# Performance work log

Hardware: AMD Instinct MI355X
Metric: run time of the kernel (lower is better)

The kernel has to match this reference:

```python
import jax, jax.numpy as jnp
import numpy as np

B, T, DEMO = 64, 4096, 8
N_MOD, N_POS = 37, 10
D_IN = N_POS + 1 + N_MOD  # 48
PHI_W, LATENT = 128, 128
PSI_W, PSI_L = 128, 128
DOT, HEADS = 64, 4
RHO_W, OUT = 128, 1
MAX_TIME = 1000.0


def _dense_init(key, fan_in, fan_out):
    lim = float(np.sqrt(6.0 / fan_in))  # he_uniform-ish
    return jax.random.uniform(key, (fan_in, fan_out), jnp.float32, -lim, lim)


def setup_inputs() -> dict:
    key = jax.random.key(0)
    ks = jax.random.split(key, 32)
    inp = {}
    inp['demo'] = jax.random.normal(ks[0], (B, DEMO), jnp.float32)
    inp['times'] = jax.random.uniform(ks[1], (B, T, 1), jnp.float32, 0.0, 100.0)
    inp['values'] = jax.random.normal(ks[2], (B, T, 1), jnp.float32)
    inp['measurements'] = jax.random.randint(ks[3], (B, T), 0, N_MOD, jnp.int32)
    # all sequences full length -> N = B*(T+1) static
    inp['segment_ids'] = jnp.repeat(jnp.arange(B, dtype=jnp.int32), T + 1)
    inp['timescales'] = jnp.asarray(MAX_TIME ** np.linspace(0.0, 1.0, N_POS // 2), jnp.float32)
    inp['demo_W1'] = _dense_init(ks[4], DEMO, PHI_W); inp['demo_b1'] = jnp.zeros((PHI_W,), jnp.float32)
    inp['demo_W2'] = _dense_init(ks[5], PHI_W, D_IN); inp['demo_b2'] = jnp.zeros((D_IN,), jnp.float32)
    dims = [D_IN, PHI_W, PHI_W, PHI_W, LATENT]
    for i in range(4):
        inp['phi_W%d' % i] = _dense_init(ks[6 + i], dims[i], dims[i + 1])
        inp['phi_b%d' % i] = jnp.zeros((dims[i + 1],), jnp.float32)
    pdims = [D_IN, PSI_W, PSI_W, PSI_L]
    for i in range(3):
        inp['psi_W%d' % i] = _dense_init(ks[10 + i], pdims[i], pdims[i + 1])
        inp['psi_b%d' % i] = jnp.zeros((pdims[i + 1],), jnp.float32)
    inp['W_k'] = _dense_init(ks[13], PSI_L + D_IN, DOT * HEADS)
    # original inits W_q to zeros (degenerate uniform attention); small random keeps test non-trivial
    inp['W_q'] = jax.random.normal(ks[14], (HEADS, DOT), jnp.float32) * 0.05
    rdims = [LATENT * HEADS, RHO_W, RHO_W, RHO_W, OUT]
    for i in range(4):
        inp['rho_W%d' % i] = _dense_init(ks[15 + i], rdims[i], rdims[i + 1])
        inp['rho_b%d' % i] = jnp.zeros((rdims[i + 1],), jnp.float32)
    return inp


def _forward(demo, times, values, timescales,
             demo_W1, demo_b1, demo_W2, demo_b2,
             phi_W0, phi_b0, phi_W1, phi_b1, phi_W2, phi_b2, phi_W3, phi_b3,
             psi_W0, psi_b0, psi_W1, psi_b1, psi_W2, psi_b2,
             W_k, W_q,
             rho_W0, rho_b0, rho_W1, rho_b1, rho_W2, rho_b2, rho_W3, rho_b3,
             measurements, segment_ids):
    relu = jax.nn.relu
    nseg = demo.shape[0]
    # positional encoding: times [B,T,1] / timescales [5] -> sin|cos -> [B,T,10]
    scaled = times / timescales[None, None, :]
    tt = jnp.concatenate([jnp.sin(scaled), jnp.cos(scaled)], axis=-1)
    meas = jax.nn.one_hot(measurements, N_MOD, dtype=times.dtype)  # [B,T,37]
    combined = jnp.concatenate([tt, values, meas], axis=-1)        # [B,T,48]
    demo_enc = relu(demo @ demo_W1 + demo_b1) @ demo_W2 + demo_b2  # [B,48]
    x = jnp.concatenate([demo_enc[:, None, :], combined], axis=1)  # [B,T+1,48]
    collected = x.reshape(-1, x.shape[-1])                         # [N,48]
    # phi MLP -> encoded [N,LATENT]
    h = collected
    for W, b in ((phi_W0, phi_b0), (phi_W1, phi_b1), (phi_W2, phi_b2), (phi_W3, phi_b3)):
        h = relu(h @ W + b)
    encoded = h
    # psi MLP -> [N,PSI_L], then per-segment mean, scattered back
    p = collected
    for W, b in ((psi_W0, psi_b0), (psi_W1, psi_b1), (psi_W2, psi_b2)):
        p = relu(p @ W + b)
    seg_sum = jax.ops.segment_sum(p, segment_ids, num_segments=nseg)
    counts = jax.ops.segment_sum(jnp.ones((p.shape[0],), p.dtype), segment_ids, num_segments=nseg)
    agg = seg_sum / counts[:, None]
    comb2 = jnp.concatenate([collected, agg[segment_ids]], axis=-1)  # [N, 48+128]
    keys = (comb2 @ W_k).reshape(-1, HEADS, DOT)                     # [N,H,D]
    preattn = jnp.einsum('nhd,hd->nh', keys, W_q) / jnp.sqrt(jnp.float32(DOT))
    # segment softmax per head
    m = jax.ops.segment_max(preattn, segment_ids, num_segments=nseg)
    e = jnp.exp(preattn - m[segment_ids])
    s = jax.ops.segment_sum(e, segment_ids, num_segments=nseg)
    attn = e / s[segment_ids]                                        # [N,H]
    # head-major weighted concat: [N, H*LATENT]
    weighted = (attn[:, :, None] * encoded[:, None, :]).reshape(-1, HEADS * LATENT)
    agg_out = jax.ops.segment_sum(weighted, segment_ids, num_segments=nseg)  # [B,512]
    r = agg_out
    for W, b in ((rho_W0, rho_b0), (rho_W1, rho_b1), (rho_W2, rho_b2)):
        r = relu(r @ W + b)
    return jax.nn.sigmoid(r @ rho_W3 + rho_b3)  # [B,1]


def reference(demo, times, values, timescales,
              demo_W1, demo_b1, demo_W2, demo_b2,
              phi_W0, phi_b0, phi_W1, phi_b1, phi_W2, phi_b2, phi_W3, phi_b3,
              psi_W0, psi_b0, psi_W1, psi_b1, psi_W2, psi_b2,
              W_k, W_q,
              rho_W0, rho_b0, rho_W1, rho_b1, rho_W2, rho_b2, rho_W3, rho_b3,
              measurements, segment_ids):
    return _forward(demo, times, values, timescales,
                    demo_W1, demo_b1, demo_W2, demo_b2,
                    phi_W0, phi_b0, phi_W1, phi_b1, phi_W2, phi_b2, phi_W3, phi_b3,
                    psi_W0, psi_b0, psi_W1, psi_b1, psi_W2, psi_b2,
                    W_k, W_q,
                    rho_W0, rho_b0, rho_W1, rho_b1, rho_W2, rho_b2, rho_W3, rho_b3,
                    measurements, segment_ids)
```

## Files before the change

### kernel.cpp

```cpp
#include <hip/hip_runtime.h>
#include <hip/hip_bf16.h>
#include <math.h>


#define BSEG 64
#define TLEN 4096
#define NPART 9
#define PART_STRIDE 520

#define OFF_DEMO 0
#define OFF_WQ   3072
#define OFF_WT   3264
#define OFF_PARTIALS 31936

typedef __attribute__((ext_vector_type(8))) short short8;
typedef __attribute__((ext_vector_type(4))) float f32x4;

static __device__ __forceinline__ float bfbits2f(unsigned v) { return __uint_as_float(v << 16); }
static __device__ __forceinline__ unsigned short f2bf_rne(float x) {
  unsigned u = __float_as_uint(x);
  unsigned r = (u + 0x7FFFu + ((u >> 16) & 1u)) >> 16;
  return (unsigned short)r;
}
static __device__ __forceinline__ unsigned pk2(float a, float b) {
  float2 f2 = make_float2(a, b);
  __hip_bfloat162 h = __float22bfloat162_rn(f2);
  unsigned u;
  __builtin_memcpy(&u, &h, 4);
  return u;
}

__global__ __launch_bounds__(256) void k_prep(
    const float* __restrict__ demo, const float* __restrict__ dW1, const float* __restrict__ db1,
    const float* __restrict__ dW2, const float* __restrict__ db2,
    const float* __restrict__ Wk, const float* __restrict__ Wq,
    const float* __restrict__ W0, const float* __restrict__ W1,
    const float* __restrict__ W2, const float* __restrict__ W3,
    float* __restrict__ ws) {
  __shared__ float drow[8];
  __shared__ float hdrow[128];
  int bid = blockIdx.x, tid = threadIdx.x;
  if (bid < 224) {
    unsigned short* wt = (unsigned short*)(ws + OFF_WT);
    int i = bid * 256 + tid;
    float v;
    if (i < 8192) {
      int n = i >> 6, k = i & 63;
      v = (k < 48) ? W0[k * 128 + n] : 0.f;
    } else {
      int j = i - 8192;
      int l = j >> 14, r = j & 16383;
      int n = r >> 7, k = r & 127;
      const float* W = (l == 0) ? W1 : (l == 1) ? W2 : W3;
      v = W[k * 128 + n];
    }
    wt[i] = f2bf_rne(v);
    return;
  }
  if (bid == 224) {
    if (tid < 192) {
      int i = tid >> 2, h = tid & 3;
      float a = 0.f;
      for (int d = 0; d < 64; ++d) a = fmaf(Wk[i * 256 + h * 64 + d], Wq[h * 64 + d], a);
      ws[OFF_WQ + tid] = a * 0.125f;
    }
    return;
  }
  int r = bid - 225;
  if (tid < 8) drow[tid] = demo[r * 8 + tid];
  __syncthreads();
  if (tid < 128) {
    float a = db1[tid];
#pragma unroll
    for (int i = 0; i < 8; ++i) a = fmaf(drow[i], dW1[i * 128 + tid], a);
    hdrow[tid] = fmaxf(a, 0.f);
  }
  __syncthreads();
  if (tid < 48) {
    float a = db2[tid];
    for (int k = 0; k < 128; ++k) a = fmaf(hdrow[k], dW2[k * 48 + tid], a);
    ws[OFF_DEMO + r * 48 + tid] = a;
  }
}

template<int MT>
static __device__ __forceinline__ void mfma_layer_T(
    const unsigned short* hin, unsigned short* hout,
    const short8 (&Wf)[2][4], const f32x4 (&bias4)[2],
    int l16, int quad, int n0) {
#pragma unroll
  for (int mt = 0; mt < MT; ++mt) {
    short8 Bv[4];
#pragma unroll
    for (int s = 0; s < 4; ++s)
      Bv[s] = *(const short8*)(hin + (mt * 16 + l16) * 136 + s * 32 + quad * 8);
    f32x4 a0 = bias4[0], a1 = bias4[1];
#pragma unroll
    for (int s = 0; s < 4; ++s) {
      a0 = __builtin_amdgcn_mfma_f32_16x16x32_bf16(Wf[0][s], Bv[s], a0, 0, 0, 0);
      a1 = __builtin_amdgcn_mfma_f32_16x16x32_bf16(Wf[1][s], Bv[s], a1, 0, 0, 0);
    }
    uint4 o;
    o.x = pk2(fmaxf(a0[0], 0.f), fmaxf(a0[1], 0.f));
    o.y = pk2(fmaxf(a0[2], 0.f), fmaxf(a0[3], 0.f));
    o.z = pk2(fmaxf(a1[0], 0.f), fmaxf(a1[1], 0.f));
    o.w = pk2(fmaxf(a1[2], 0.f), fmaxf(a1[3], 0.f));
    *(uint4*)(hout + (mt * 16 + l16) * 136 + n0 + quad * 8) = o;
  }
}
template<int MT>
static __device__ __forceinline__ void mfma_layer0_T(
    const unsigned short* cin, unsigned short* hout,
    const short8 (&Wf)[2][2], const f32x4 (&bias4)[2],
    int l16, int quad, int n0) {
#pragma unroll
  for (int mt = 0; mt < MT; ++mt) {
    short8 Bv[2];
#pragma unroll
    for (int s = 0; s < 2; ++s)
      Bv[s] = *(const short8*)(cin + (mt * 16 + l16) * 72 + s * 32 + quad * 8);
    f32x4 a0 = bias4[0], a1 = bias4[1];
    a0 = __builtin_amdgcn_mfma_f32_16x16x32_bf16(Wf[0][0], Bv[0], a0, 0, 0, 0);
    a0 = __builtin_amdgcn_mfma_f32_16x16x32_bf16(Wf[0][1], Bv[1], a0, 0, 0, 0);
    a1 = __builtin_amdgcn_mfma_f32_16x16x32_bf16(Wf[1][0], Bv[0], a1, 0, 0, 0);
    a1 = __builtin_amdgcn_mfma_f32_16x16x32_bf16(Wf[1][1], Bv[1], a1, 0, 0, 0);
    uint4 o;
    o.x = pk2(fmaxf(a0[0], 0.f), fmaxf(a0[1], 0.f));
    o.y = pk2(fmaxf(a0[2], 0.f), fmaxf(a0[3], 0.f));
    o.z = pk2(fmaxf(a1[0], 0.f), fmaxf(a1[1], 0.f));
    o.w = pk2(fmaxf(a1[2], 0.f), fmaxf(a1[3], 0.f));
    *(uint4*)(hout + (mt * 16 + l16) * 136 + n0 + quad * 8) = o;
  }
}

__global__ __launch_bounds__(256, 2) void k_main(
    const float* __restrict__ times, const float* __restrict__ values,
    const int* __restrict__ meas, const float* __restrict__ tsc,
    const float* __restrict__ ws,
    const float* __restrict__ b0g, const float* __restrict__ b1g,
    const float* __restrict__ b2g, const float* __restrict__ b3g,
    float* __restrict__ part) {
  __shared__ __align__(16) unsigned short hA[128 * 136];
  __shared__ __align__(16) unsigned short hB[128 * 136];
  __shared__ __align__(16) float preb[512 * 4];
  __shared__ float wql[192];
  __shared__ float mred[16];
  int tid = threadIdx.x;
  const int lane = tid & 63, wv = tid >> 6, quad = lane >> 4, l16 = lane & 15;
  const int n0 = wv * 32;

  const unsigned short* wt = (const unsigned short*)(ws + OFF_WT);
  short8 B0[2][2], B1[2][4], B2[2][4], B3[2][4];
  f32x4 bias0[2], bias1[2], bias2[2];
  float bias3[2];
#pragma unroll
  for (int t = 0; t < 2; ++t) {
    int n  = n0 + ((l16 >> 2) << 3) + t * 4 + (l16 & 3);
    int nq = n0 + quad * 8 + t * 4;
    bias0[t] = *(const f32x4*)(b0g + nq);
    bias1[t] = *(const f32x4*)(b1g + nq);
    bias2[t] = *(const f32x4*)(b2g + nq);
    bias3[t] = b3g[n];
#pragma unroll
    for (int s = 0; s < 2; ++s)
      B0[t][s] = *(const short8*)(wt + n * 64 + s * 32 + quad * 8);
#pragma unroll
    for (int s = 0; s < 4; ++s) {
      B1[t][s] = *(const short8*)(wt + 8192  + n * 128 + s * 32 + quad * 8);
      B2[t][s] = *(const short8*)(wt + 24576 + n * 128 + s * 32 + quad * 8);
      B3[t][s] = *(const short8*)(wt + 40960 + n * 128 + s * 32 + quad * 8);
    }
  }
  if (tid < 192) wql[tid] = ws[OFF_WQ + tid];
  __syncthreads();

  if (blockIdx.x == 512) {
    {
      int r = tid >> 2, cs = tid & 3;
      unsigned short seg[16];
#pragma unroll
      for (int i = 0; i < 16; ++i) seg[i] = 0;
      if (cs < 3)
#pragma unroll
        for (int i = 0; i < 16; ++i) seg[i] = f2bf_rne(ws[OFF_DEMO + r * 48 + cs * 16 + i]);
      unsigned u[8];
#pragma unroll
      for (int i = 0; i < 8; ++i) u[i] = (unsigned)seg[2 * i] | ((unsigned)seg[2 * i + 1] << 16);
      uint4* dst = (uint4*)(hB + r * 72 + cs * 16);
      dst[0] = make_uint4(u[0], u[1], u[2], u[3]);
      dst[1] = make_uint4(u[4], u[5], u[6], u[7]);
    }
    {
      int r = tid >> 2, h = tid & 3;
      float a = 0.f;
      for (int i = 0; i < 48; ++i) a = fmaf(ws[OFF_DEMO + r * 48 + i], wql[i * 4 + h], a);
      preb[tid] = __expf(a);
    }
    f32x4 bias34[2];
#pragma unroll
    for (int t = 0; t < 2; ++t) bias34[t] = *(const f32x4*)(b3g + n0 + quad * 8 + t * 4);
    __syncthreads();
    mfma_layer0_T<4>(hB, hA, B0, bias0, l16, quad, n0); __syncthreads();
    mfma_layer_T<4>(hA, hB, B1, bias1, l16, quad, n0); __syncthreads();
    mfma_layer_T<4>(hB, hA, B2, bias2, l16, quad, n0); __syncthreads();
    mfma_layer_T<4>(hA, hB, B3, bias34, l16, quad, n0); __syncthreads();
    {
      int r = tid >> 2, h = tid & 3;
      part[(r * NPART + 8) * PART_STRIDE + 4 + h] = preb[tid];
    }
    for (int i = tid; i < 64 * 512; i += 256) {
      int r = i >> 9, rem = i & 511;
      int h = rem >> 7, l = rem & 127;
      part[(r * NPART + 8) * PART_STRIDE + 8 + rem] =
          preb[r * 4 + h] * bfbits2f(hB[r * 136 + l]);
    }
    return;
  }

  int b = blockIdx.x >> 3, c = blockIdx.x & 7;
  int t0 = c << 9;
  float invts[5];
#pragma unroll
  for (int i = 0; i < 5; ++i) invts[i] = 1.f / tsc[i];

  float s4[4] = {0.f, 0.f, 0.f, 0.f};
  unsigned usv0[8], usv1[8];
#pragma unroll
  for (int rr = 0; rr < 2; ++rr) {
    int r = tid + rr * 256;
    int t = t0 + r;
    float tv = times[b * TLEN + t];
    float vvv = values[b * TLEN + t];
    int mm = meas[b * TLEN + t];
    float f[11];
#pragma unroll
    for (int i = 0; i < 5; ++i) { float s = tv * invts[i]; f[i] = __sinf(s); f[5 + i] = __cosf(s); }
    f[10] = vvv;
#pragma unroll
    for (int h = 0; h < 4; ++h) {
      float a = wql[(11 + mm) * 4 + h];
#pragma unroll
      for (int i = 0; i < 11; ++i) a = fmaf(f[i], wql[i * 4 + h], a);
      float e = __expf(a);
      preb[r * 4 + h] = e;
      s4[h] += e;
    }
    int kk = 11 + mm;
    unsigned uu[8];
    uu[0] = pk2(f[0], f[1]); uu[1] = pk2(f[2], f[3]);
    uu[2] = pk2(f[4], f[5]); uu[3] = pk2(f[6], f[7]);
    uu[4] = pk2(f[8], f[9]);
    uu[5] = pk2(f[10], (kk == 11) ? 1.f : 0.f);
    uu[6] = ((kk == 12) ? 0x3F80u : 0u) | ((kk == 13) ? 0x3F800000u : 0u);
    uu[7] = ((kk == 14) ? 0x3F80u : 0u) | ((kk == 15) ? 0x3F800000u : 0u);
    if (rr == 0) {
#pragma unroll
      for (int k = 0; k < 8; ++k) usv0[k] = uu[k];
    } else {
#pragma unroll
      for (int k = 0; k < 8; ++k) usv1[k] = uu[k];
    }
  }

  auto build_tile = [&](int tile) {
    int r = tid & 127;
    if (((tid >> 7) & 1) == (tile & 1)) {
      unsigned uw[8];
#pragma unroll
      for (int k = 0; k < 8; ++k) uw[k] = (tile & 2) ? usv1[k] : usv0[k];
      uint4* dst = (uint4*)(hB + r * 72);
      dst[0] = make_uint4(uw[0], uw[1], uw[2], uw[3]);
      dst[1] = make_uint4(uw[4], uw[5], uw[6], uw[7]);
    } else {
      int t = t0 + tile * 128 + r;
      int mm = meas[b * TLEN + t];
      int kk = 11 + mm;
      uint4 z = make_uint4(0u, 0u, 0u, 0u);
      uint4* dst = (uint4*)(hB + r * 72 + 16);
#pragma unroll
      for (int k = 0; k < 6; ++k) dst[k] = z;
      asm volatile("" ::: "memory");
      if (kk >= 16) hB[r * 72 + kk] = 0x3F80;
    }
  };

  float pacc[2][4] = {{0.f, 0.f, 0.f, 0.f}, {0.f, 0.f, 0.f, 0.f}};
  const int ncb = n0 + ((l16 >> 2) << 3) + (l16 & 3);
  build_tile(0);
  for (int tile = 0; tile < 4; ++tile) {
    int rb = tile << 7;
    __syncthreads();
    mfma_layer0_T<8>(hB, hA, B0, bias0, l16, quad, n0); __syncthreads();
    mfma_layer_T<8>(hA, hB, B1, bias1, l16, quad, n0); __syncthreads();
    mfma_layer_T<8>(hB, hA, B2, bias2, l16, quad, n0); __syncthreads();
    if (tile < 3) build_tile(tile + 1);
#pragma unroll
    for (int mt = 0; mt < 8; ++mt) {
      short8 A[4];
#pragma unroll
      for (int s = 0; s < 4; ++s)
        A[s] = *(const short8*)(hA + (mt * 16 + l16) * 136 + s * 32 + quad * 8);
      f32x4 acc0 = {bias3[0], bias3[0], bias3[0], bias3[0]};
      f32x4 acc1 = {bias3[1], bias3[1], bias3[1], bias3[1]};
#pragma unroll
      for (int s = 0; s < 4; ++s) {
        acc0 = __builtin_amdgcn_mfma_f32_16x16x32_bf16(A[s], B3[0][s], acc0, 0, 0, 0);
        acc1 = __builtin_amdgcn_mfma_f32_16x16x32_bf16(A[s], B3[1][s], acc1, 0, 0, 0);
      }
#pragma unroll
      for (int j = 0; j < 4; ++j) {
        int row = rb + mt * 16 + quad * 4 + j;
        float4 e4 = *(const float4*)(preb + row * 4);
        float v0 = fmaxf(acc0[j], 0.f), v1 = fmaxf(acc1[j], 0.f);
        pacc[0][0] = fmaf(v0, e4.x, pacc[0][0]);
        pacc[0][1] = fmaf(v0, e4.y, pacc[0][1]);
        pacc[0][2] = fmaf(v0, e4.z, pacc[0][2]);
        pacc[0][3] = fmaf(v0, e4.w, pacc[0][3]);
        pacc[1][0] = fmaf(v1, e4.x, pacc[1][0]);
        pacc[1][1] = fmaf(v1, e4.y, pacc[1][1]);
        pacc[1][2] = fmaf(v1, e4.z, pacc[1][2]);
        pacc[1][3] = fmaf(v1, e4.w, pacc[1][3]);
      }
    }
  }
#pragma unroll
  for (int t = 0; t < 2; ++t)
#pragma unroll
    for (int h = 0; h < 4; ++h) {
      float v = pacc[t][h];
      v += __shfl_xor(v, 16, 64);
      v += __shfl_xor(v, 32, 64);
      pacc[t][h] = v;
    }
#pragma unroll
  for (int off = 32; off > 0; off >>= 1)
#pragma unroll
    for (int h = 0; h < 4; ++h) s4[h] += __shfl_xor(s4[h], off, 64);
  if (lane == 0)
#pragma unroll
    for (int h = 0; h < 4; ++h) mred[wv * 4 + h] = s4[h];
  __syncthreads();
  float* P = part + (b * NPART + c) * PART_STRIDE;
  if (tid < 4) P[4 + tid] = mred[tid] + mred[4 + tid] + mred[8 + tid] + mred[12 + tid];
  if (quad == 0)
#pragma unroll
    for (int t = 0; t < 2; ++t)
#pragma unroll
      for (int h = 0; h < 4; ++h)
        P[8 + h * 128 + (ncb + t * 4)] = pacc[t][h];
}

__global__ __launch_bounds__(256) void k_combine(
    const float* __restrict__ part,
    const float* __restrict__ rW0, const float* __restrict__ rb0,
    const float* __restrict__ rW1, const float* __restrict__ rb1,
    const float* __restrict__ rW2, const float* __restrict__ rb2,
    const float* __restrict__ rW3, const float* __restrict__ rb3,
    float* __restrict__ out) {
  __shared__ float Ss[4], agg[512], r1[128], p0[256];
  int tid = threadIdx.x;
  int b = blockIdx.x;
  const float* P = part + b * NPART * PART_STRIDE;
  if (tid < 4) {
    float s = 0.f;
    for (int p = 0; p < NPART; ++p) s += P[p * PART_STRIDE + 4 + tid];
    Ss[tid] = s;
  }
  __syncthreads();
  for (int idx = tid; idx < 512; idx += 256) {
    int h = idx >> 7;
    float a = 0.f;
    for (int p = 0; p < NPART; ++p) a += P[p * PART_STRIDE + 8 + idx];
    agg[idx] = a / Ss[h];
  }
  __syncthreads();
  const int col = tid & 127, half = tid >> 7;
  {
    float a = 0.f;
    for (int k = half * 256; k < half * 256 + 256; ++k) a = fmaf(agg[k], rW0[k * 128 + col], a);
    p0[tid] = a;
  }
  __syncthreads();
  if (tid < 128) r1[tid] = fmaxf(rb0[tid] + p0[tid] + p0[128 + tid], 0.f);
  __syncthreads();
  {
    float a = 0.f;
    for (int k = half * 64; k < half * 64 + 64; ++k) a = fmaf(r1[k], rW1[k * 128 + col], a);
    p0[tid] = a;
  }
  __syncthreads();
  if (tid < 128) r1[tid] = fmaxf(rb1[tid] + p0[tid] + p0[128 + tid], 0.f);
  __syncthreads();
  {
    float a = 0.f;
    for (int k = half * 64; k < half * 64 + 64; ++k) a = fmaf(r1[k], rW2[k * 128 + col], a);
    p0[tid] = a;
  }
  __syncthreads();
  if (tid < 128) p0[tid] = fmaxf(rb2[tid] + p0[tid] + p0[128 + tid], 0.f) * rW3[tid];
  __syncthreads();
  if (tid < 64) {
    float v = p0[tid] + p0[tid + 64];
#pragma unroll
    for (int off = 32; off > 0; off >>= 1) v += __shfl_xor(v, off, 64);
    if (tid == 0) out[b] = 1.f / (1.f + __expf(-(rb3[0] + v)));
  }
}

extern "C" void kernel_launch(void* const* d_in, const int* in_sizes, int n_in,
                              void* d_out, int out_size, void* d_ws, size_t ws_size,
                              hipStream_t stream) {
  const float* demo   = (const float*)d_in[0];
  const float* times  = (const float*)d_in[1];
  const float* values = (const float*)d_in[2];
  const int*   meas   = (const int*)d_in[3];
  const float* tsc = (const float*)d_in[5];
  const float* dW1 = (const float*)d_in[6];
  const float* db1 = (const float*)d_in[7];
  const float* dW2 = (const float*)d_in[8];
  const float* db2 = (const float*)d_in[9];
  const float* pW0 = (const float*)d_in[10];
  const float* pb0 = (const float*)d_in[11];
  const float* pW1 = (const float*)d_in[12];
  const float* pb1 = (const float*)d_in[13];
  const float* pW2 = (const float*)d_in[14];
  const float* pb2 = (const float*)d_in[15];
  const float* pW3 = (const float*)d_in[16];
  const float* pb3 = (const float*)d_in[17];
  const float* Wk  = (const float*)d_in[24];
  const float* Wq  = (const float*)d_in[25];
  const float* rW0 = (const float*)d_in[26];
  const float* rb0 = (const float*)d_in[27];
  const float* rW1 = (const float*)d_in[28];
  const float* rb1 = (const float*)d_in[29];
  const float* rW2 = (const float*)d_in[30];
  const float* rb2 = (const float*)d_in[31];
  const float* rW3 = (const float*)d_in[32];
  const float* rb3 = (const float*)d_in[33];
  float* ws = (float*)d_ws;
  float* partials = ws + OFF_PARTIALS;

  k_prep<<<289, 256, 0, stream>>>(demo, dW1, db1, dW2, db2, Wk, Wq,
                                  pW0, pW1, pW2, pW3, ws);
  k_main<<<513, 256, 0, stream>>>(times, values, meas, tsc, ws,
                                  pb0, pb1, pb2, pb3, partials);
  k_combine<<<64, 256, 0, stream>>>(partials, rW0, rb0, rW1, rb1, rW2, rb2, rW3, rb3,
                                    (float*)d_out);
}
```

Measured before the change: 183.1 us.

## Add MFMA priority hints, vectorize epilogues, and trim redundant LDS zeroing

```diff
diff --git a/kernel.cpp b/kernel.cpp
--- a/kernel.cpp
+++ b/kernel.cpp
@@ -15,6 +15,7 @@
 
 typedef __attribute__((ext_vector_type(8))) short short8;
 typedef __attribute__((ext_vector_type(4))) float f32x4;
+typedef __attribute__((ext_vector_type(2))) float f32x2;
 
 static __device__ __forceinline__ float bfbits2f(unsigned v) { return __uint_as_float(v << 16); }
 static __device__ __forceinline__ unsigned short f2bf_rne(float x) {
@@ -88,6 +89,7 @@
     const unsigned short* hin, unsigned short* hout,
     const short8 (&Wf)[2][4], const f32x4 (&bias4)[2],
     int l16, int quad, int n0) {
+  const f32x4 z4 = {0.f, 0.f, 0.f, 0.f};
 #pragma unroll
   for (int mt = 0; mt < MT; ++mt) {
     short8 Bv[4];
@@ -95,16 +97,20 @@
     for (int s = 0; s < 4; ++s)
       Bv[s] = *(const short8*)(hin + (mt * 16 + l16) * 136 + s * 32 + quad * 8);
     f32x4 a0 = bias4[0], a1 = bias4[1];
+    __builtin_amdgcn_s_setprio(1);
 #pragma unroll
     for (int s = 0; s < 4; ++s) {
       a0 = __builtin_amdgcn_mfma_f32_16x16x32_bf16(Wf[0][s], Bv[s], a0, 0, 0, 0);
       a1 = __builtin_amdgcn_mfma_f32_16x16x32_bf16(Wf[1][s], Bv[s], a1, 0, 0, 0);
     }
+    __builtin_amdgcn_s_setprio(0);
+    f32x4 r0 = __builtin_elementwise_max(a0, z4);
+    f32x4 r1 = __builtin_elementwise_max(a1, z4);
     uint4 o;
-    o.x = pk2(fmaxf(a0[0], 0.f), fmaxf(a0[1], 0.f));
-    o.y = pk2(fmaxf(a0[2], 0.f), fmaxf(a0[3], 0.f));
-    o.z = pk2(fmaxf(a1[0], 0.f), fmaxf(a1[1], 0.f));
-    o.w = pk2(fmaxf(a1[2], 0.f), fmaxf(a1[3], 0.f));
+    o.x = pk2(r0[0], r0[1]);
+    o.y = pk2(r0[2], r0[3]);
+    o.z = pk2(r1[0], r1[1]);
+    o.w = pk2(r1[2], r1[3]);
     *(uint4*)(hout + (mt * 16 + l16) * 136 + n0 + quad * 8) = o;
   }
 }
@@ -113,6 +119,7 @@
     const unsigned short* cin, unsigned short* hout,
     const short8 (&Wf)[2][2], const f32x4 (&bias4)[2],
     int l16, int quad, int n0) {
+  const f32x4 z4 = {0.f, 0.f, 0.f, 0.f};
 #pragma unroll
   for (int mt = 0; mt < MT; ++mt) {
     short8 Bv[2];
@@ -120,15 +127,19 @@
     for (int s = 0; s < 2; ++s)
       Bv[s] = *(const short8*)(cin + (mt * 16 + l16) * 72 + s * 32 + quad * 8);
     f32x4 a0 = bias4[0], a1 = bias4[1];
+    __builtin_amdgcn_s_setprio(1);
     a0 = __builtin_amdgcn_mfma_f32_16x16x32_bf16(Wf[0][0], Bv[0], a0, 0, 0, 0);
     a0 = __builtin_amdgcn_mfma_f32_16x16x32_bf16(Wf[0][1], Bv[1], a0, 0, 0, 0);
     a1 = __builtin_amdgcn_mfma_f32_16x16x32_bf16(Wf[1][0], Bv[0], a1, 0, 0, 0);
     a1 = __builtin_amdgcn_mfma_f32_16x16x32_bf16(Wf[1][1], Bv[1], a1, 0, 0, 0);
+    __builtin_amdgcn_s_setprio(0);
+    f32x4 r0 = __builtin_elementwise_max(a0, z4);
+    f32x4 r1 = __builtin_elementwise_max(a1, z4);
     uint4 o;
-    o.x = pk2(fmaxf(a0[0], 0.f), fmaxf(a0[1], 0.f));
-    o.y = pk2(fmaxf(a0[2], 0.f), fmaxf(a0[3], 0.f));
-    o.z = pk2(fmaxf(a1[0], 0.f), fmaxf(a1[1], 0.f));
-    o.w = pk2(fmaxf(a1[2], 0.f), fmaxf(a1[3], 0.f));
+    o.x = pk2(r0[0], r0[1]);
+    o.y = pk2(r0[2], r0[3]);
+    o.z = pk2(r1[0], r1[1]);
+    o.w = pk2(r1[2], r1[3]);
     *(uint4*)(hout + (mt * 16 + l16) * 136 + n0 + quad * 8) = o;
   }
 }
@@ -143,7 +154,7 @@
   __shared__ __align__(16) unsigned short hA[128 * 136];
   __shared__ __align__(16) unsigned short hB[128 * 136];
   __shared__ __align__(16) float preb[512 * 4];
-  __shared__ float wql[192];
+  __shared__ __align__(16) float wql[192];
   __shared__ float mred[16];
   int tid = threadIdx.x;
   const int lane = tid & 63, wv = tid >> 6, quad = lane >> 4, l16 = lane & 15;
@@ -225,6 +236,7 @@
 
   float s4[4] = {0.f, 0.f, 0.f, 0.f};
   unsigned usv0[8], usv1[8];
+  const f32x4* wql4 = (const f32x4*)wql;
 #pragma unroll
   for (int rr = 0; rr < 2; ++rr) {
     int r = tid + rr * 256;
@@ -236,15 +248,16 @@
 #pragma unroll
     for (int i = 0; i < 5; ++i) { float s = tv * invts[i]; f[i] = __sinf(s); f[5 + i] = __cosf(s); }
     f[10] = vvv;
-#pragma unroll
-    for (int h = 0; h < 4; ++h) {
-      float a = wql[(11 + mm) * 4 + h];
-#pragma unroll
-      for (int i = 0; i < 11; ++i) a = fmaf(f[i], wql[i * 4 + h], a);
-      float e = __expf(a);
-      preb[r * 4 + h] = e;
-      s4[h] += e;
-    }
+    f32x4 a4 = wql4[11 + mm];
+#pragma unroll
+    for (int i = 0; i < 11; ++i) {
+      f32x4 fi = {f[i], f[i], f[i], f[i]};
+      a4 = __builtin_elementwise_fma(fi, wql4[i], a4);
+    }
+    float e0 = __expf(a4[0]), e1 = __expf(a4[1]);
+    float e2 = __expf(a4[2]), e3 = __expf(a4[3]);
+    *(f32x4*)(preb + r * 4) = (f32x4){e0, e1, e2, e3};
+    s4[0] += e0; s4[1] += e1; s4[2] += e2; s4[3] += e3;
     int kk = 11 + mm;
     unsigned uu[8];
     uu[0] = pk2(f[0], f[1]); uu[1] = pk2(f[2], f[3]);
@@ -271,6 +284,9 @@
       uint4* dst = (uint4*)(hB + r * 72);
       dst[0] = make_uint4(uw[0], uw[1], uw[2], uw[3]);
       dst[1] = make_uint4(uw[4], uw[5], uw[6], uw[7]);
+      uint4 z = make_uint4(0u, 0u, 0u, 0u);
+      *(uint4*)(hB + r * 72 + 48) = z;
+      *(uint4*)(hB + r * 72 + 56) = z;
     } else {
       int t = t0 + tile * 128 + r;
       int mm = meas[b * TLEN + t];
@@ -278,13 +294,14 @@
       uint4 z = make_uint4(0u, 0u, 0u, 0u);
       uint4* dst = (uint4*)(hB + r * 72 + 16);
 #pragma unroll
-      for (int k = 0; k < 6; ++k) dst[k] = z;
+      for (int k = 0; k < 4; ++k) dst[k] = z;
       asm volatile("" ::: "memory");
       if (kk >= 16) hB[r * 72 + kk] = 0x3F80;
     }
   };
 
-  float pacc[2][4] = {{0.f, 0.f, 0.f, 0.f}, {0.f, 0.f, 0.f, 0.f}};
+  f32x2 pacc2[2][2] = {{{0.f, 0.f}, {0.f, 0.f}}, {{0.f, 0.f}, {0.f, 0.f}}};
+  const f32x4 z4 = {0.f, 0.f, 0.f, 0.f};
   const int ncb = n0 + ((l16 >> 2) << 3) + (l16 & 3);
   build_tile(0);
   for (int tile = 0; tile < 4; ++tile) {
@@ -302,27 +319,33 @@
         A[s] = *(const short8*)(hA + (mt * 16 + l16) * 136 + s * 32 + quad * 8);
       f32x4 acc0 = {bias3[0], bias3[0], bias3[0], bias3[0]};
       f32x4 acc1 = {bias3[1], bias3[1], bias3[1], bias3[1]};
+      __builtin_amdgcn_s_setprio(1);
 #pragma unroll
       for (int s = 0; s < 4; ++s) {
         acc0 = __builtin_amdgcn_mfma_f32_16x16x32_bf16(A[s], B3[0][s], acc0, 0, 0, 0);
         acc1 = __builtin_amdgcn_mfma_f32_16x16x32_bf16(A[s], B3[1][s], acc1, 0, 0, 0);
       }
+      __builtin_amdgcn_s_setprio(0);
+      f32x4 r0 = __builtin_elementwise_max(acc0, z4);
+      f32x4 r1 = __builtin_elementwise_max(acc1, z4);
 #pragma unroll
       for (int j = 0; j < 4; ++j) {
         int row = rb + mt * 16 + quad * 4 + j;
-        float4 e4 = *(const float4*)(preb + row * 4);
-        float v0 = fmaxf(acc0[j], 0.f), v1 = fmaxf(acc1[j], 0.f);
-        pacc[0][0] = fmaf(v0, e4.x, pacc[0][0]);
-        pacc[0][1] = fmaf(v0, e4.y, pacc[0][1]);
-        pacc[0][2] = fmaf(v0, e4.z, pacc[0][2]);
-        pacc[0][3] = fmaf(v0, e4.w, pacc[0][3]);
-        pacc[1][0] = fmaf(v1, e4.x, pacc[1][0]);
-        pacc[1][1] = fmaf(v1, e4.y, pacc[1][1]);
-        pacc[1][2] = fmaf(v1, e4.z, pacc[1][2]);
-        pacc[1][3] = fmaf(v1, e4.w, pacc[1][3]);
+        f32x4 e4 = *(const f32x4*)(preb + row * 4);
+        f32x2 e01 = {e4[0], e4[1]}, e23 = {e4[2], e4[3]};
+        f32x2 v0 = {r0[j], r0[j]}, v1 = {r1[j], r1[j]};
+        pacc2[0][0] = __builtin_elementwise_fma(v0, e01, pacc2[0][0]);
+        pacc2[0][1] = __builtin_elementwise_fma(v0, e23, pacc2[0][1]);
+        pacc2[1][0] = __builtin_elementwise_fma(v1, e01, pacc2[1][0]);
+        pacc2[1][1] = __builtin_elementwise_fma(v1, e23, pacc2[1][1]);
       }
     }
   }
+  float pacc[2][4];
+#pragma unroll
+  for (int t = 0; t < 2; ++t)
+#pragma unroll
+    for (int h = 0; h < 4; ++h) pacc[t][h] = pacc2[t][h >> 1][h & 1];
 #pragma unroll
   for (int t = 0; t < 2; ++t)
 #pragma unroll
```

Result: no change. 183.3 us (median of 2 runs) (+0.1%).
